# Optimization experiments

Hardware: AMD Instinct MI355X
Metric: run time of the kernel (lower is better)

The kernel has to match this reference:

```python
import jax, jax.numpy as jnp
import numpy as np

B, S, D, H = 1, 2048, 768, 12
HD = D // H


def layer_norm(x, g, b, eps=1e-5):
    mu = x.mean(-1, keepdims=True)
    var = ((x - mu) ** 2).mean(-1, keepdims=True)
    return (x - mu) * jax.lax.rsqrt(var + eps) * g + b


def setup_inputs() -> dict:
    key = jax.random.key(0)
    ks = jax.random.split(key, 16)
    s = 0.02
    exp_encodings = jax.random.normal(ks[0], (B, S, D), dtype=jnp.float32)
    pert_encodings = jax.random.normal(ks[1], (B, S, D), dtype=jnp.float32)
    adj = (jax.random.uniform(ks[2], (S, S)) < 0.01).astype(jnp.int32)
    adj = adj.at[jnp.arange(S), jnp.arange(S)].set(1)
    in_proj_w = jax.random.normal(ks[3], (3 * D, D)) * s
    in_proj_b = jnp.zeros((3 * D,), jnp.float32)
    out_proj_w = jax.random.normal(ks[4], (D, D)) * s
    out_proj_b = jnp.zeros((D,), jnp.float32)
    ln0_g = jnp.ones((D,), jnp.float32); ln0_b = jnp.zeros((D,), jnp.float32)
    ln1_g = jnp.ones((D,), jnp.float32); ln1_b = jnp.zeros((D,), jnp.float32)
    ln2_g = jnp.ones((D,), jnp.float32); ln2_b = jnp.zeros((D,), jnp.float32)
    w1 = jax.random.normal(ks[5], (D // 2, D)) * s
    b1 = jnp.zeros((D // 2,), jnp.float32)
    w2 = jax.random.normal(ks[6], (D, D // 2)) * s
    b2 = jnp.zeros((D,), jnp.float32)
    return dict(exp_encodings=exp_encodings, pert_encodings=pert_encodings,
                in_proj_w=in_proj_w, in_proj_b=in_proj_b,
                out_proj_w=out_proj_w, out_proj_b=out_proj_b,
                ln0_g=ln0_g, ln0_b=ln0_b, ln1_g=ln1_g, ln1_b=ln1_b,
                ln2_g=ln2_g, ln2_b=ln2_b, w1=w1, b1=b1, w2=w2, b2=b2,
                adj=adj)


def reference(exp_encodings, pert_encodings, in_proj_w, in_proj_b,
              out_proj_w, out_proj_b, ln0_g, ln0_b, ln1_g, ln1_b,
              ln2_g, ln2_b, w1, b1, w2, b2, adj):
    b, s, d = exp_encodings.shape
    hd = d // H
    # additive mask: 0 where edge, -inf elsewhere (diag guaranteed edge)
    mask = jnp.where(adj > 0, 0.0, -jnp.inf).astype(exp_encodings.dtype)
    x_in = layer_norm(exp_encodings + pert_encodings, ln0_g, ln0_b)
    # torch MultiheadAttention (batch_first) self-attention
    qkv = x_in @ in_proj_w.T + in_proj_b          # [b,s,3d]
    q, k, v = jnp.split(qkv, 3, axis=-1)
    q = q.reshape(b, s, H, hd)
    k = k.reshape(b, s, H, hd)
    v = v.reshape(b, s, H, hd)
    scores = jnp.einsum('bqhe,bkhe->bhqk', q, k) / np.sqrt(hd) + mask
    attn = jax.nn.softmax(scores, axis=-1)
    o = jnp.einsum('bhqk,bkhe->bqhe', attn, v).reshape(b, s, d)
    o = o @ out_proj_w.T + out_proj_b
    x = layer_norm(o + x_in, ln1_g, ln1_b)
    ff = jax.nn.relu(x @ w1.T + b1) @ w2.T + b2
    return layer_norm(x + ff, ln2_g, ln2_b)
```

## Files before the change

kernel.cpp:

```cpp
#include <hip/hip_runtime.h>

#define S 2048
#define D 768
#define NH 12
#define HD 64
#define TD (3 * D)

typedef __bf16 bf16_t;
typedef __bf16 v8bf __attribute__((ext_vector_type(8)));
typedef __bf16 v4bf __attribute__((ext_vector_type(4)));
typedef float v4f __attribute__((ext_vector_type(4)));

__device__ __forceinline__ float wave_reduce_sum(float v) {
#pragma unroll
    for (int o = 32; o > 0; o >>= 1) v += __shfl_down(v, o, 64);
    return v;
}
__device__ float block_reduce_sum(float v) {
    __shared__ float t4[4];
    int lane = threadIdx.x & 63, wid = threadIdx.x >> 6;
    v = wave_reduce_sum(v);
    __syncthreads();
    if (lane == 0) t4[wid] = v;
    __syncthreads();
    return t4[0] + t4[1] + t4[2] + t4[3];
}

#define NW0 (TD * D / 4)
#define NW1 (D * D / 4)
#define NW2 ((D / 2) * D / 4)
#define NW3 (D * (D / 2) / 4)
#define NWALL (NW0 + NW1 + NW2 + NW3)

__global__ __launch_bounds__(256) void addln_cvt(const float* __restrict__ A, const float* __restrict__ Bv,
                                                 const float* __restrict__ g, const float* __restrict__ be,
                                                 bf16_t* __restrict__ out,
                                                 const float* __restrict__ s0, const float* __restrict__ s1,
                                                 const float* __restrict__ s2, const float* __restrict__ s3,
                                                 bf16_t* __restrict__ d0, bf16_t* __restrict__ d1,
                                                 bf16_t* __restrict__ d2, bf16_t* __restrict__ d3) {
    int blk = blockIdx.x, t = threadIdx.x;
    if (blk >= S) {
        int i = (blk - S) * 256 + t;
        const float* sp; bf16_t* dp;
        if (i < NW0) { sp = s0; dp = d0; }
        else if (i < NW0 + NW1) { sp = s1; dp = d1; i -= NW0; }
        else if (i < NW0 + NW1 + NW2) { sp = s2; dp = d2; i -= NW0 + NW1; }
        else if (i < NWALL) { sp = s3; dp = d3; i -= NW0 + NW1 + NW2; }
        else return;
        float4 v = ((const float4*)sp)[i];
        v4bf o = {(bf16_t)v.x, (bf16_t)v.y, (bf16_t)v.z, (bf16_t)v.w};
        *(v4bf*)(dp + (size_t)i * 4) = o;
        return;
    }
    int row = blk;
    const float* a = A + (size_t)row * D;
    const float* b = Bv + (size_t)row * D;
    float x[3];
    float s = 0.f;
#pragma unroll
    for (int i = 0; i < 3; ++i) { int c = t + 256 * i; x[i] = a[c] + b[c]; s += x[i]; }
    float mean = block_reduce_sum(s) * (1.0f / D);
    float vs = 0.f;
#pragma unroll
    for (int i = 0; i < 3; ++i) { float d = x[i] - mean; vs += d * d; }
    float var = block_reduce_sum(vs) * (1.0f / D);
    float rstd = rsqrtf(var + 1e-5f);
#pragma unroll
    for (int i = 0; i < 3; ++i) {
        int c = t + 256 * i;
        out[(size_t)row * D + c] = (bf16_t)((x[i] - mean) * rstd * g[c] + be[c]);
    }
}

template <typename TO>
__global__ __launch_bounds__(256) void ln_only(const bf16_t* __restrict__ X,
                                               const float* __restrict__ g, const float* __restrict__ be,
                                               TO* __restrict__ out) {
    int row = blockIdx.x, t = threadIdx.x;
    const bf16_t* a = X + (size_t)row * D;
    float x[3];
    float s = 0.f;
#pragma unroll
    for (int i = 0; i < 3; ++i) { int c = t + 256 * i; x[i] = (float)a[c]; s += x[i]; }
    float mean = block_reduce_sum(s) * (1.0f / D);
    float vs = 0.f;
#pragma unroll
    for (int i = 0; i < 3; ++i) { float d = x[i] - mean; vs += d * d; }
    float var = block_reduce_sum(vs) * (1.0f / D);
    float rstd = rsqrtf(var + 1e-5f);
#pragma unroll
    for (int i = 0; i < 3; ++i) {
        int c = t + 256 * i;
        out[(size_t)row * D + c] = (TO)((x[i] - mean) * rstd * g[c] + be[c]);
    }
}

#define GBK 64

template <int TM, int TN, int RELU, bool RESID>
__global__ __launch_bounds__(256) void gemm_mfma(const bf16_t* __restrict__ A, const bf16_t* __restrict__ B,
                                                 const float* __restrict__ bias,
                                                 const bf16_t* __restrict__ Rsd, bf16_t* __restrict__ C,
                                                 int M, int N, int K) {
    constexpr int CA = TM * 8;
    constexpr int CHUNKS = (TM + TN) * 8;
    constexpr int P = CHUNKS / 256;
    static_assert(CHUNKS % 256 == 0, "chunk passes must be exact");
    constexpr int MI = TM / 32, NI = TN / 32;
    __shared__ bf16_t As[TM * GBK];
    __shared__ bf16_t Bs[TN * GBK];
    const int t = threadIdx.x;
    const int lane = t & 63, wave = t >> 6;
    const int wr = (wave >> 1) * (TM / 2), wc = (wave & 1) * (TN / 2);
    const int m0 = blockIdx.y * TM, n0 = blockIdx.x * TN;
    const int lm = lane & 15, q = lane >> 4;

    const bf16_t* gsrc[P];
    bf16_t* ldst[P];
#pragma unroll
    for (int p = 0; p < P; ++p) {
        int c = t + 256 * p;
        if (c < CA) {
            int slab = c / (TM * 4), r4 = c % (TM * 4);
            int row = r4 >> 2, c4 = r4 & 3;
            gsrc[p] = A + (size_t)(m0 + row) * K + slab * 32 + c4 * 8;
            ldst[p] = As + slab * (TM * 32) + row * 32 + c4 * 8;
        } else {
            int cc = c - CA;
            int slab = cc / (TN * 4), r4 = cc % (TN * 4);
            int row = r4 >> 2, c4 = r4 & 3;
            gsrc[p] = B + (size_t)(n0 + row) * K + slab * 32 + c4 * 8;
            ldst[p] = Bs + slab * (TN * 32) + row * 32 + c4 * 8;
        }
    }

    v4f acc[MI][NI] = {};

    for (int k0 = 0; k0 < K; k0 += GBK) {
#pragma unroll
        for (int p = 0; p < P; ++p)
            __builtin_amdgcn_global_load_lds((const __attribute__((address_space(1))) void*)(gsrc[p] + k0),
                                             (__attribute__((address_space(3))) void*)ldst[p], 16, 0, 0);
        __syncthreads();

        v8bf af[2][MI], bfr[2][NI];
#pragma unroll
        for (int s = 0; s < 2; ++s) {
#pragma unroll
            for (int i = 0; i < MI; ++i)
                af[s][i] = *(const v8bf*)(As + s * (TM * 32) + (wr + i * 16 + lm) * 32 + q * 8);
#pragma unroll
            for (int j = 0; j < NI; ++j)
                bfr[s][j] = *(const v8bf*)(Bs + s * (TN * 32) + (wc + j * 16 + lm) * 32 + q * 8);
        }
#pragma unroll
        for (int s = 0; s < 2; ++s)
#pragma unroll
            for (int i = 0; i < MI; ++i)
#pragma unroll
                for (int j = 0; j < NI; ++j)
                    acc[i][j] = __builtin_amdgcn_mfma_f32_16x16x32_bf16(af[s][i], bfr[s][j], acc[i][j], 0, 0, 0);
        __syncthreads();
    }

#pragma unroll
    for (int i = 0; i < MI; ++i)
#pragma unroll
        for (int j = 0; j < NI; ++j) {
            int col = n0 + wc + j * 16 + lm;
            float bs = bias[col];
#pragma unroll
            for (int r = 0; r < 4; ++r) {
                int row = m0 + wr + i * 16 + q * 4 + r;
                float v = acc[i][j][r] + bs;
                if (RELU) v = fmaxf(v, 0.f);
                if (RESID) v += (float)Rsd[(size_t)row * N + col];
                C[(size_t)row * N + col] = (bf16_t)v;
            }
        }
}

__global__ __launch_bounds__(256) void attn_sparse(const bf16_t* __restrict__ qkv, const int* __restrict__ adj,
                                                   bf16_t* __restrict__ O) {
    __shared__ int s_idx[128];
    __shared__ int s_cnt;
    __shared__ float s_q[D];
    __shared__ float s_p[NH][128];

    const int row = blockIdx.x, t = threadIdx.x;
    const int lane = t & 63, wave = t >> 6;
    if (t == 0) s_cnt = 0;
    __syncthreads();

    const int4* arow = (const int4*)(adj + (size_t)row * S);
#pragma unroll
    for (int p = 0; p < 2; ++p) {
        int4 v = arow[t + 256 * p];
        int base = (t + 256 * p) * 4;
        if (v.x) { int k = atomicAdd(&s_cnt, 1); if (k < 128) s_idx[k] = base + 0; }
        if (v.y) { int k = atomicAdd(&s_cnt, 1); if (k < 128) s_idx[k] = base + 1; }
        if (v.z) { int k = atomicAdd(&s_cnt, 1); if (k < 128) s_idx[k] = base + 2; }
        if (v.w) { int k = atomicAdd(&s_cnt, 1); if (k < 128) s_idx[k] = base + 3; }
    }
    for (int c = t; c < D; c += 256) s_q[c] = (float)qkv[(size_t)row * TD + c];
    __syncthreads();
    const int n = (s_cnt < 128) ? s_cnt : 128;

    for (int it = t; it < n * NH; it += 256) {
        int h = it / n, i = it - h * n;
        int j = s_idx[i];
        const bf16_t* kp = qkv + (size_t)j * TD + D + h * HD;
        const float* qp = s_q + h * HD;
        float dot = 0.f;
#pragma unroll
        for (int c = 0; c < HD; c += 8) {
            v8bf kv = *(const v8bf*)(kp + c);
#pragma unroll
            for (int e = 0; e < 8; ++e) dot += qp[c + e] * (float)kv[e];
        }
        s_p[h][i] = dot * 0.125f;
    }
    __syncthreads();

    for (int h = wave; h < NH; h += 4) {
        float v0 = (lane < n) ? s_p[h][lane] : -1e30f;
        float v1 = (lane + 64 < n) ? s_p[h][lane + 64] : -1e30f;
        float m = fmaxf(v0, v1);
#pragma unroll
        for (int o = 32; o > 0; o >>= 1) m = fmaxf(m, __shfl_xor(m, o, 64));
        float p0 = (lane < n) ? __expf(v0 - m) : 0.f;
        float p1 = (lane + 64 < n) ? __expf(v1 - m) : 0.f;
        float sm = p0 + p1;
#pragma unroll
        for (int o = 32; o > 0; o >>= 1) sm += __shfl_xor(sm, o, 64);
        float inv = 1.f / sm;
        if (lane < n) s_p[h][lane] = p0 * inv;
        if (lane + 64 < n) s_p[h][lane + 64] = p1 * inv;
    }
    __syncthreads();

    for (int o = t; o < D; o += 256) {
        int h = o >> 6, e = o & 63;
        const float* pp = s_p[h];
        float acc = 0.f;
        for (int i = 0; i < n; ++i)
            acc += pp[i] * (float)qkv[(size_t)s_idx[i] * TD + 2 * D + h * HD + e];
        O[(size_t)row * D + o] = (bf16_t)acc;
    }
}

extern "C" void kernel_launch(void* const* d_in, const int* in_sizes, int n_in,
                              void* d_out, int out_size, void* d_ws, size_t ws_size,
                              hipStream_t stream) {
    const float* exp_e = (const float*)d_in[0];
    const float* pert  = (const float*)d_in[1];
    const float* w_in  = (const float*)d_in[2];
    const float* b_in  = (const float*)d_in[3];
    const float* w_out = (const float*)d_in[4];
    const float* b_out = (const float*)d_in[5];
    const float* g0  = (const float*)d_in[6];
    const float* be0 = (const float*)d_in[7];
    const float* g1  = (const float*)d_in[8];
    const float* be1 = (const float*)d_in[9];
    const float* g2  = (const float*)d_in[10];
    const float* be2 = (const float*)d_in[11];
    const float* w1  = (const float*)d_in[12];
    const float* b1  = (const float*)d_in[13];
    const float* w2  = (const float*)d_in[14];
    const float* b2  = (const float*)d_in[15];
    const int*   adj = (const int*)d_in[16];
    float* out = (float*)d_out;

    const size_t SD = (size_t)S * D;
    bf16_t* wb_in  = (bf16_t*)d_ws;
    bf16_t* wb_out = wb_in + (size_t)TD * D;
    bf16_t* wb_1   = wb_out + (size_t)D * D;
    bf16_t* wb_2   = wb_1 + (size_t)(D / 2) * D;
    bf16_t* x_in   = wb_2 + (size_t)D * (D / 2);
    bf16_t* qkv    = x_in + SD;
    bf16_t* attn_o = qkv + 3 * SD;
    bf16_t* y1     = attn_o + SD;
    bf16_t* x1     = y1 + SD;
    bf16_t* ffh    = x1 + SD;
    bf16_t* y2     = ffh + SD / 2;

    const int CVTB = (NWALL + 255) / 256;
    addln_cvt<<<S + CVTB, 256, 0, stream>>>(exp_e, pert, g0, be0, x_in,
                                            w_in, w_out, w1, w2, wb_in, wb_out, wb_1, wb_2);
    gemm_mfma<64, 128, 0, false><<<dim3(TD / 128, S / 64), 256, 0, stream>>>(x_in, wb_in, b_in, nullptr, qkv, S, TD, D);
    attn_sparse<<<S, 256, 0, stream>>>(qkv, adj, attn_o);
    gemm_mfma<64, 64, 0, true><<<dim3(D / 64, S / 64), 256, 0, stream>>>(attn_o, wb_out, b_out, x_in, y1, S, D, D);
    ln_only<bf16_t><<<S, 256, 0, stream>>>(y1, g1, be1, x1);
    gemm_mfma<32, 64, 1, false><<<dim3((D / 2) / 64, S / 32), 256, 0, stream>>>(x1, wb_1, b1, nullptr, ffh, S, D / 2, D);
    gemm_mfma<64, 64, 0, true><<<dim3(D / 64, S / 64), 256, 0, stream>>>(ffh, wb_2, b2, x1, y2, S, D, D / 2);
    ln_only<float><<<S, 256, 0, stream>>>(y2, g2, be2, out);
}
```

Baseline: 196.3 us.

## Fuse LayerNorm into FF1 GEMM and unroll sparse attention dot/accumulate loops

Adds a kernel that computes LayerNorm of each 32-row tile directly into shared memory and then runs the first feed-forward GEMM with ReLU from that tile. This removes the separate ln_only launch and the reload of x1 from global memory. Only the blockIdx.x==0 column of blocks writes x1 out for the residual. The cost is that the LayerNorm is recomputed in each of the six N-tile blocks. The sparse attention kernel also gets vectorized float4 q loads in the QK dot and four independent accumulators in the PV gather, to expose more memory-level parallelism.

After: 203.6 us. 3.7% more time.

```diff
diff --git a/kernel.cpp b/kernel.cpp
--- a/kernel.cpp
+++ b/kernel.cpp
@@ -181,6 +181,96 @@
         }
 }
 
+#define FTM 32
+#define FTN 64
+#define FK  768
+#define FN  384
+
+__global__ __launch_bounds__(256) void ff1_ln_gemm(const bf16_t* __restrict__ y1,
+                                                   const float* __restrict__ g, const float* __restrict__ be,
+                                                   const bf16_t* __restrict__ B, const float* __restrict__ bias,
+                                                   bf16_t* __restrict__ x1g, bf16_t* __restrict__ Cffh) {
+    __shared__ bf16_t x1s[24 * 32 * 32];
+    __shared__ bf16_t Bs[FTN * GBK];
+    const int t = threadIdx.x, lane = t & 63, wave = t >> 6;
+    const int m0 = blockIdx.y * FTM, n0 = blockIdx.x * FTN;
+    const int lm = lane & 15, q = lane >> 4;
+
+#pragma unroll
+    for (int rr = 0; rr < 8; ++rr) {
+        int row = wave * 8 + rr;
+        const bf16_t* yp = y1 + (size_t)(m0 + row) * D;
+        float v[12];
+        float s = 0.f, s2 = 0.f;
+#pragma unroll
+        for (int e = 0; e < 12; ++e) {
+            v[e] = (float)yp[lane + 64 * e];
+            s += v[e]; s2 += v[e] * v[e];
+        }
+#pragma unroll
+        for (int o = 32; o > 0; o >>= 1) { s += __shfl_xor(s, o, 64); s2 += __shfl_xor(s2, o, 64); }
+        float mean = s * (1.0f / D);
+        float var = s2 * (1.0f / D) - mean * mean;
+        float rstd = rsqrtf(var + 1e-5f);
+#pragma unroll
+        for (int e = 0; e < 12; ++e) {
+            int c = lane + 64 * e;
+            bf16_t xv = (bf16_t)((v[e] - mean) * rstd * g[c] + be[c]);
+            x1s[(c >> 5) * 1024 + row * 32 + (c & 31)] = xv;
+            if (blockIdx.x == 0) x1g[(size_t)(m0 + row) * D + c] = xv;
+        }
+    }
+    __syncthreads();
+
+    const bf16_t* gsrc[2];
+    bf16_t* ldst[2];
+#pragma unroll
+    for (int p = 0; p < 2; ++p) {
+        int c = t + 256 * p;
+        int slab = c >> 8, r4 = c & 255;
+        int row = r4 >> 2, c4 = r4 & 3;
+        gsrc[p] = B + (size_t)(n0 + row) * FK + slab * 32 + c4 * 8;
+        ldst[p] = Bs + slab * (FTN * 32) + row * 32 + c4 * 8;
+    }
+
+    v4f acc[2] = {};
+    const int wr = (wave >> 1) * 16, wc = (wave & 1) * 32;
+
+    for (int k0 = 0; k0 < FK; k0 += GBK) {
+#pragma unroll
+        for (int p = 0; p < 2; ++p)
+            __builtin_amdgcn_global_load_lds((const __attribute__((address_space(1))) void*)(gsrc[p] + k0),
+                                             (__attribute__((address_space(3))) void*)ldst[p], 16, 0, 0);
+        __syncthreads();
+
+        v8bf af[2], bfr[2][2];
+#pragma unroll
+        for (int s = 0; s < 2; ++s) {
+            af[s] = *(const v8bf*)(x1s + ((k0 >> 5) + s) * 1024 + (wr + lm) * 32 + q * 8);
+#pragma unroll
+            for (int j = 0; j < 2; ++j)
+                bfr[s][j] = *(const v8bf*)(Bs + s * (FTN * 32) + (wc + j * 16 + lm) * 32 + q * 8);
+        }
+#pragma unroll
+        for (int s = 0; s < 2; ++s)
+#pragma unroll
+            for (int j = 0; j < 2; ++j)
+                acc[j] = __builtin_amdgcn_mfma_f32_16x16x32_bf16(af[s], bfr[s][j], acc[j], 0, 0, 0);
+        __syncthreads();
+    }
+
+#pragma unroll
+    for (int j = 0; j < 2; ++j) {
+        int col = n0 + wc + j * 16 + lm;
+        float bs = bias[col];
+#pragma unroll
+        for (int r = 0; r < 4; ++r) {
+            int row = m0 + wr + q * 4 + r;
+            Cffh[(size_t)row * FN + col] = (bf16_t)fmaxf(acc[j][r] + bs, 0.f);
+        }
+    }
+}
+
 __global__ __launch_bounds__(256) void attn_sparse(const bf16_t* __restrict__ qkv, const int* __restrict__ adj,
                                                    bf16_t* __restrict__ O) {
     __shared__ int s_idx[128];
@@ -210,14 +300,15 @@
     for (int it = t; it < n * NH; it += 256) {
         int h = it / n, i = it - h * n;
         int j = s_idx[i];
-        const bf16_t* kp = qkv + (size_t)j * TD + D + h * HD;
-        const float* qp = s_q + h * HD;
+        const v8bf* kp = (const v8bf*)(qkv + (size_t)j * TD + D + h * HD);
+        const float4* qp = (const float4*)(s_q + h * HD);
         float dot = 0.f;
 #pragma unroll
-        for (int c = 0; c < HD; c += 8) {
-            v8bf kv = *(const v8bf*)(kp + c);
-#pragma unroll
-            for (int e = 0; e < 8; ++e) dot += qp[c + e] * (float)kv[e];
+        for (int c = 0; c < 8; ++c) {
+            v8bf kv = kp[c];
+            float4 qa = qp[2 * c], qb = qp[2 * c + 1];
+            dot += qa.x * (float)kv[0] + qa.y * (float)kv[1] + qa.z * (float)kv[2] + qa.w * (float)kv[3]
+                 + qb.x * (float)kv[4] + qb.y * (float)kv[5] + qb.z * (float)kv[6] + qb.w * (float)kv[7];
         }
         s_p[h][i] = dot * 0.125f;
     }
@@ -243,10 +334,18 @@
     for (int o = t; o < D; o += 256) {
         int h = o >> 6, e = o & 63;
         const float* pp = s_p[h];
-        float acc = 0.f;
-        for (int i = 0; i < n; ++i)
-            acc += pp[i] * (float)qkv[(size_t)s_idx[i] * TD + 2 * D + h * HD + e];
-        O[(size_t)row * D + o] = (bf16_t)acc;
+        const bf16_t* vbase = qkv + 2 * D + h * HD + e;
+        float a0 = 0.f, a1 = 0.f, a2 = 0.f, a3 = 0.f;
+        int i = 0;
+        for (; i + 4 <= n; i += 4) {
+            int j0 = s_idx[i], j1 = s_idx[i + 1], j2 = s_idx[i + 2], j3 = s_idx[i + 3];
+            a0 += pp[i]     * (float)vbase[(size_t)j0 * TD];
+            a1 += pp[i + 1] * (float)vbase[(size_t)j1 * TD];
+            a2 += pp[i + 2] * (float)vbase[(size_t)j2 * TD];
+            a3 += pp[i + 3] * (float)vbase[(size_t)j3 * TD];
+        }
+        for (; i < n; ++i) a0 += pp[i] * (float)vbase[(size_t)s_idx[i] * TD];
+        O[(size_t)row * D + o] = (bf16_t)((a0 + a1) + (a2 + a3));
     }
 }
 
@@ -291,8 +390,7 @@
     gemm_mfma<64, 128, 0, false><<<dim3(TD / 128, S / 64), 256, 0, stream>>>(x_in, wb_in, b_in, nullptr, qkv, S, TD, D);
     attn_sparse<<<S, 256, 0, stream>>>(qkv, adj, attn_o);
     gemm_mfma<64, 64, 0, true><<<dim3(D / 64, S / 64), 256, 0, stream>>>(attn_o, wb_out, b_out, x_in, y1, S, D, D);
-    ln_only<bf16_t><<<S, 256, 0, stream>>>(y1, g1, be1, x1);
-    gemm_mfma<32, 64, 1, false><<<dim3((D / 2) / 64, S / 32), 256, 0, stream>>>(x1, wb_1, b1, nullptr, ffh, S, D / 2, D);
+    ff1_ln_gemm<<<dim3(FN / FTN, S / FTM), 256, 0, stream>>>(y1, g1, be1, wb_1, b1, x1, ffh);
     gemm_mfma<64, 64, 0, true><<<dim3(D / 64, S / 64), 256, 0, stream>>>(ffh, wb_2, b2, x1, y2, S, D, D / 2);
     ln_only<float><<<S, 256, 0, stream>>>(y2, g2, be2, out);
 }
```

## Replace tiled GEMM with B-resident kernel reading A from global, vectorize attention

Applied to the files above, without the earlier changes.

The shared-memory double-operand tiled GEMM is replaced by a kernel that loads a full 32-column slice of the weight matrix (all of K) into LDS once, then streams A fragments directly from global memory into MFMA with no per-K-step barriers. Each block covers CH*32 rows, so launch shapes change for all four GEMMs. The attention kernel also uses float4 loads of q in the score loop and four independent accumulators in the value gather to expose more memory-level parallelism. The cost is uncoalesced, uncached-in-LDS A reads that rely on L2 reuse across blocks, and large LDS per block for K=768 (48KB), which can limit occupancy.

New measurement: 255.2 us. 1.3x slower.

```diff
diff --git a/kernel.cpp b/kernel.cpp
--- a/kernel.cpp
+++ b/kernel.cpp
@@ -96,89 +96,56 @@
     }
 }
 
-#define GBK 64
-
-template <int TM, int TN, int RELU, bool RESID>
-__global__ __launch_bounds__(256) void gemm_mfma(const bf16_t* __restrict__ A, const bf16_t* __restrict__ B,
+template <int N, int K, int CH, int RELU, bool RESID>
+__global__ __launch_bounds__(256) void gemm_bres(const bf16_t* __restrict__ A, const bf16_t* __restrict__ B,
                                                  const float* __restrict__ bias,
-                                                 const bf16_t* __restrict__ Rsd, bf16_t* __restrict__ C,
-                                                 int M, int N, int K) {
-    constexpr int CA = TM * 8;
-    constexpr int CHUNKS = (TM + TN) * 8;
-    constexpr int P = CHUNKS / 256;
-    static_assert(CHUNKS % 256 == 0, "chunk passes must be exact");
-    constexpr int MI = TM / 32, NI = TN / 32;
-    __shared__ bf16_t As[TM * GBK];
-    __shared__ bf16_t Bs[TN * GBK];
-    const int t = threadIdx.x;
-    const int lane = t & 63, wave = t >> 6;
-    const int wr = (wave >> 1) * (TM / 2), wc = (wave & 1) * (TN / 2);
-    const int m0 = blockIdx.y * TM, n0 = blockIdx.x * TN;
+                                                 const bf16_t* __restrict__ Rsd, bf16_t* __restrict__ C) {
+    constexpr int SLABS = K / 32;
+    constexpr int PASSES = SLABS * 128 / 256;
+    __shared__ bf16_t Bs[SLABS * 1024];
+    const int t = threadIdx.x, lane = t & 63, wave = t >> 6;
+    const int wm = wave >> 1, wn = wave & 1;
     const int lm = lane & 15, q = lane >> 4;
-
-    const bf16_t* gsrc[P];
-    bf16_t* ldst[P];
-#pragma unroll
-    for (int p = 0; p < P; ++p) {
+    const int n0 = blockIdx.x * 32;
+    const int m0 = blockIdx.y * (CH * 32);
+
+#pragma unroll
+    for (int p = 0; p < PASSES; ++p) {
         int c = t + 256 * p;
-        if (c < CA) {
-            int slab = c / (TM * 4), r4 = c % (TM * 4);
-            int row = r4 >> 2, c4 = r4 & 3;
-            gsrc[p] = A + (size_t)(m0 + row) * K + slab * 32 + c4 * 8;
-            ldst[p] = As + slab * (TM * 32) + row * 32 + c4 * 8;
-        } else {
-            int cc = c - CA;
-            int slab = cc / (TN * 4), r4 = cc % (TN * 4);
-            int row = r4 >> 2, c4 = r4 & 3;
-            gsrc[p] = B + (size_t)(n0 + row) * K + slab * 32 + c4 * 8;
-            ldst[p] = Bs + slab * (TN * 32) + row * 32 + c4 * 8;
+        int slab = c >> 7, g = (c >> 5) & 3, r = c & 31;
+        __builtin_amdgcn_global_load_lds(
+            (const __attribute__((address_space(1))) void*)(B + (size_t)(n0 + r) * K + slab * 32 + g * 8),
+            (__attribute__((address_space(3))) void*)(Bs + c * 8), 16, 0, 0);
+    }
+    __syncthreads();
+
+    v4f acc[CH] = {};
+    const bf16_t* Ab = A + (size_t)(m0 + wm * 16 + lm) * K + q * 8;
+#pragma unroll 4
+    for (int slab = 0; slab < SLABS; ++slab) {
+        v8bf bfr = *(const v8bf*)(Bs + slab * 1024 + q * 256 + (wn * 16 + lm) * 8);
+        v8bf af[CH];
+#pragma unroll
+        for (int c = 0; c < CH; ++c)
+            af[c] = *(const v8bf*)(Ab + (size_t)(32 * c) * K + slab * 32);
+#pragma unroll
+        for (int c = 0; c < CH; ++c)
+            acc[c] = __builtin_amdgcn_mfma_f32_16x16x32_bf16(af[c], bfr, acc[c], 0, 0, 0);
+    }
+
+    const int col = n0 + wn * 16 + lm;
+    const float bb = bias[col];
+#pragma unroll
+    for (int c = 0; c < CH; ++c) {
+#pragma unroll
+        for (int r = 0; r < 4; ++r) {
+            int row = m0 + wm * 16 + 32 * c + q * 4 + r;
+            float v = acc[c][r] + bb;
+            if (RELU) v = fmaxf(v, 0.f);
+            if (RESID) v += (float)Rsd[(size_t)row * N + col];
+            C[(size_t)row * N + col] = (bf16_t)v;
         }
     }
-
-    v4f acc[MI][NI] = {};
-
-    for (int k0 = 0; k0 < K; k0 += GBK) {
-#pragma unroll
-        for (int p = 0; p < P; ++p)
-            __builtin_amdgcn_global_load_lds((const __attribute__((address_space(1))) void*)(gsrc[p] + k0),
-                                             (__attribute__((address_space(3))) void*)ldst[p], 16, 0, 0);
-        __syncthreads();
-
-        v8bf af[2][MI], bfr[2][NI];
-#pragma unroll
-        for (int s = 0; s < 2; ++s) {
-#pragma unroll
-            for (int i = 0; i < MI; ++i)
-                af[s][i] = *(const v8bf*)(As + s * (TM * 32) + (wr + i * 16 + lm) * 32 + q * 8);
-#pragma unroll
-            for (int j = 0; j < NI; ++j)
-                bfr[s][j] = *(const v8bf*)(Bs + s * (TN * 32) + (wc + j * 16 + lm) * 32 + q * 8);
-        }
-#pragma unroll
-        for (int s = 0; s < 2; ++s)
-#pragma unroll
-            for (int i = 0; i < MI; ++i)
-#pragma unroll
-                for (int j = 0; j < NI; ++j)
-                    acc[i][j] = __builtin_amdgcn_mfma_f32_16x16x32_bf16(af[s][i], bfr[s][j], acc[i][j], 0, 0, 0);
-        __syncthreads();
-    }
-
-#pragma unroll
-    for (int i = 0; i < MI; ++i)
-#pragma unroll
-        for (int j = 0; j < NI; ++j) {
-            int col = n0 + wc + j * 16 + lm;
-            float bs = bias[col];
-#pragma unroll
-            for (int r = 0; r < 4; ++r) {
-                int row = m0 + wr + i * 16 + q * 4 + r;
-                float v = acc[i][j][r] + bs;
-                if (RELU) v = fmaxf(v, 0.f);
-                if (RESID) v += (float)Rsd[(size_t)row * N + col];
-                C[(size_t)row * N + col] = (bf16_t)v;
-            }
-        }
 }
 
 __global__ __launch_bounds__(256) void attn_sparse(const bf16_t* __restrict__ qkv, const int* __restrict__ adj,
@@ -210,14 +177,15 @@
     for (int it = t; it < n * NH; it += 256) {
         int h = it / n, i = it - h * n;
         int j = s_idx[i];
-        const bf16_t* kp = qkv + (size_t)j * TD + D + h * HD;
-        const float* qp = s_q + h * HD;
+        const v8bf* kp = (const v8bf*)(qkv + (size_t)j * TD + D + h * HD);
+        const float4* qp = (const float4*)(s_q + h * HD);
         float dot = 0.f;
 #pragma unroll
-        for (int c = 0; c < HD; c += 8) {
-            v8bf kv = *(const v8bf*)(kp + c);
-#pragma unroll
-            for (int e = 0; e < 8; ++e) dot += qp[c + e] * (float)kv[e];
+        for (int c = 0; c < 8; ++c) {
+            v8bf kv = kp[c];
+            float4 qa = qp[2 * c], qb = qp[2 * c + 1];
+            dot += qa.x * (float)kv[0] + qa.y * (float)kv[1] + qa.z * (float)kv[2] + qa.w * (float)kv[3]
+                 + qb.x * (float)kv[4] + qb.y * (float)kv[5] + qb.z * (float)kv[6] + qb.w * (float)kv[7];
         }
         s_p[h][i] = dot * 0.125f;
     }
@@ -243,10 +211,18 @@
     for (int o = t; o < D; o += 256) {
         int h = o >> 6, e = o & 63;
         const float* pp = s_p[h];
-        float acc = 0.f;
-        for (int i = 0; i < n; ++i)
-            acc += pp[i] * (float)qkv[(size_t)s_idx[i] * TD + 2 * D + h * HD + e];
-        O[(size_t)row * D + o] = (bf16_t)acc;
+        const bf16_t* vbase = qkv + 2 * D + h * HD + e;
+        float a0 = 0.f, a1 = 0.f, a2 = 0.f, a3 = 0.f;
+        int i = 0;
+        for (; i + 4 <= n; i += 4) {
+            int j0 = s_idx[i], j1 = s_idx[i + 1], j2 = s_idx[i + 2], j3 = s_idx[i + 3];
+            a0 += pp[i]     * (float)vbase[(size_t)j0 * TD];
+            a1 += pp[i + 1] * (float)vbase[(size_t)j1 * TD];
+            a2 += pp[i + 2] * (float)vbase[(size_t)j2 * TD];
+            a3 += pp[i + 3] * (float)vbase[(size_t)j3 * TD];
+        }
+        for (; i < n; ++i) a0 += pp[i] * (float)vbase[(size_t)s_idx[i] * TD];
+        O[(size_t)row * D + o] = (bf16_t)((a0 + a1) + (a2 + a3));
     }
 }
 
@@ -288,11 +264,11 @@
     const int CVTB = (NWALL + 255) / 256;
     addln_cvt<<<S + CVTB, 256, 0, stream>>>(exp_e, pert, g0, be0, x_in,
                                             w_in, w_out, w1, w2, wb_in, wb_out, wb_1, wb_2);
-    gemm_mfma<64, 128, 0, false><<<dim3(TD / 128, S / 64), 256, 0, stream>>>(x_in, wb_in, b_in, nullptr, qkv, S, TD, D);
+    gemm_bres<TD, D, 4, 0, false><<<dim3(TD / 32, S / 128), 256, 0, stream>>>(x_in, wb_in, b_in, nullptr, qkv);
     attn_sparse<<<S, 256, 0, stream>>>(qkv, adj, attn_o);
-    gemm_mfma<64, 64, 0, true><<<dim3(D / 64, S / 64), 256, 0, stream>>>(attn_o, wb_out, b_out, x_in, y1, S, D, D);
+    gemm_bres<D, D, 2, 0, true><<<dim3(D / 32, S / 64), 256, 0, stream>>>(attn_o, wb_out, b_out, x_in, y1);
     ln_only<bf16_t><<<S, 256, 0, stream>>>(y1, g1, be1, x1);
-    gemm_mfma<32, 64, 1, false><<<dim3((D / 2) / 64, S / 32), 256, 0, stream>>>(x1, wb_1, b1, nullptr, ffh, S, D / 2, D);
-    gemm_mfma<64, 64, 0, true><<<dim3(D / 64, S / 64), 256, 0, stream>>>(ffh, wb_2, b2, x1, y2, S, D, D / 2);
+    gemm_bres<D / 2, D, 2, 1, false><<<dim3((D / 2) / 32, S / 64), 256, 0, stream>>>(x1, wb_1, b1, nullptr, ffh);
+    gemm_bres<D, D / 2, 2, 0, true><<<dim3(D / 32, S / 64), 256, 0, stream>>>(ffh, wb_2, b2, x1, y2);
     ln_only<float><<<S, 256, 0, stream>>>(y2, g2, be2, out);
 }
```

## Build adjacency index lists in the first kernel and unroll sparse attention loops

Applied to the files above, without the earlier changes.

The per-row scan of the adjacency matrix moves out of the attention kernel into extra blocks of the first LayerNorm/convert kernel, which write a compact index list and count per row to workspace. The attention kernel then loads only the prepared indices, so it no longer reads a 2048-int row of the mask while the QKV data sits in cache. The QK dot product now reads q with float4 loads, and the PV loop uses four independent accumulators to raise memory-level parallelism on the gathered V loads. The cost is extra workspace and more blocks in the first launch.

Result: slower. 201.8 us (+2.8%).

```diff
diff --git a/kernel.cpp b/kernel.cpp
--- a/kernel.cpp
+++ b/kernel.cpp
@@ -31,6 +31,7 @@
 #define NW2 ((D / 2) * D / 4)
 #define NW3 (D * (D / 2) / 4)
 #define NWALL (NW0 + NW1 + NW2 + NW3)
+#define CVTB ((NWALL + 255) / 256)
 
 __global__ __launch_bounds__(256) void addln_cvt(const float* __restrict__ A, const float* __restrict__ Bv,
                                                  const float* __restrict__ g, const float* __restrict__ be,
@@ -38,8 +39,32 @@
                                                  const float* __restrict__ s0, const float* __restrict__ s1,
                                                  const float* __restrict__ s2, const float* __restrict__ s3,
                                                  bf16_t* __restrict__ d0, bf16_t* __restrict__ d1,
-                                                 bf16_t* __restrict__ d2, bf16_t* __restrict__ d3) {
+                                                 bf16_t* __restrict__ d2, bf16_t* __restrict__ d3,
+                                                 const int* __restrict__ adj,
+                                                 int* __restrict__ csr_cnt, int* __restrict__ csr_idx) {
     int blk = blockIdx.x, t = threadIdx.x;
+    if (blk >= S + CVTB) {
+        __shared__ int sc_idx[128];
+        __shared__ int sc_cnt;
+        int row = blk - S - CVTB;
+        if (t == 0) sc_cnt = 0;
+        __syncthreads();
+        const int4* arow = (const int4*)(adj + (size_t)row * S);
+#pragma unroll
+        for (int p = 0; p < 2; ++p) {
+            int4 v = arow[t + 256 * p];
+            int base = (t + 256 * p) * 4;
+            if (v.x) { int k = atomicAdd(&sc_cnt, 1); if (k < 128) sc_idx[k] = base + 0; }
+            if (v.y) { int k = atomicAdd(&sc_cnt, 1); if (k < 128) sc_idx[k] = base + 1; }
+            if (v.z) { int k = atomicAdd(&sc_cnt, 1); if (k < 128) sc_idx[k] = base + 2; }
+            if (v.w) { int k = atomicAdd(&sc_cnt, 1); if (k < 128) sc_idx[k] = base + 3; }
+        }
+        __syncthreads();
+        int n = (sc_cnt < 128) ? sc_cnt : 128;
+        if (t == 0) csr_cnt[row] = n;
+        if (t < n) csr_idx[(size_t)row * 128 + t] = sc_idx[t];
+        return;
+    }
     if (blk >= S) {
         int i = (blk - S) * 256 + t;
         const float* sp; bf16_t* dp;
@@ -181,43 +206,34 @@
         }
 }
 
-__global__ __launch_bounds__(256) void attn_sparse(const bf16_t* __restrict__ qkv, const int* __restrict__ adj,
+__global__ __launch_bounds__(256) void attn_sparse(const bf16_t* __restrict__ qkv,
+                                                   const int* __restrict__ csr_cnt,
+                                                   const int* __restrict__ csr_idx,
                                                    bf16_t* __restrict__ O) {
     __shared__ int s_idx[128];
-    __shared__ int s_cnt;
     __shared__ float s_q[D];
     __shared__ float s_p[NH][128];
 
     const int row = blockIdx.x, t = threadIdx.x;
     const int lane = t & 63, wave = t >> 6;
-    if (t == 0) s_cnt = 0;
-    __syncthreads();
-
-    const int4* arow = (const int4*)(adj + (size_t)row * S);
-#pragma unroll
-    for (int p = 0; p < 2; ++p) {
-        int4 v = arow[t + 256 * p];
-        int base = (t + 256 * p) * 4;
-        if (v.x) { int k = atomicAdd(&s_cnt, 1); if (k < 128) s_idx[k] = base + 0; }
-        if (v.y) { int k = atomicAdd(&s_cnt, 1); if (k < 128) s_idx[k] = base + 1; }
-        if (v.z) { int k = atomicAdd(&s_cnt, 1); if (k < 128) s_idx[k] = base + 2; }
-        if (v.w) { int k = atomicAdd(&s_cnt, 1); if (k < 128) s_idx[k] = base + 3; }
-    }
+    const int n = csr_cnt[row];
+
+    if (t < n) s_idx[t] = csr_idx[(size_t)row * 128 + t];
     for (int c = t; c < D; c += 256) s_q[c] = (float)qkv[(size_t)row * TD + c];
     __syncthreads();
-    const int n = (s_cnt < 128) ? s_cnt : 128;
 
     for (int it = t; it < n * NH; it += 256) {
         int h = it / n, i = it - h * n;
         int j = s_idx[i];
-        const bf16_t* kp = qkv + (size_t)j * TD + D + h * HD;
-        const float* qp = s_q + h * HD;
+        const v8bf* kp = (const v8bf*)(qkv + (size_t)j * TD + D + h * HD);
+        const float4* qp = (const float4*)(s_q + h * HD);
         float dot = 0.f;
 #pragma unroll
-        for (int c = 0; c < HD; c += 8) {
-            v8bf kv = *(const v8bf*)(kp + c);
-#pragma unroll
-            for (int e = 0; e < 8; ++e) dot += qp[c + e] * (float)kv[e];
+        for (int c = 0; c < 8; ++c) {
+            v8bf kv = kp[c];
+            float4 qa = qp[2 * c], qb = qp[2 * c + 1];
+            dot += qa.x * (float)kv[0] + qa.y * (float)kv[1] + qa.z * (float)kv[2] + qa.w * (float)kv[3]
+                 + qb.x * (float)kv[4] + qb.y * (float)kv[5] + qb.z * (float)kv[6] + qb.w * (float)kv[7];
         }
         s_p[h][i] = dot * 0.125f;
     }
@@ -243,10 +259,18 @@
     for (int o = t; o < D; o += 256) {
         int h = o >> 6, e = o & 63;
         const float* pp = s_p[h];
-        float acc = 0.f;
-        for (int i = 0; i < n; ++i)
-            acc += pp[i] * (float)qkv[(size_t)s_idx[i] * TD + 2 * D + h * HD + e];
-        O[(size_t)row * D + o] = (bf16_t)acc;
+        const bf16_t* vbase = qkv + 2 * D + h * HD + e;
+        float a0 = 0.f, a1 = 0.f, a2 = 0.f, a3 = 0.f;
+        int i = 0;
+        for (; i + 4 <= n; i += 4) {
+            int j0 = s_idx[i], j1 = s_idx[i + 1], j2 = s_idx[i + 2], j3 = s_idx[i + 3];
+            a0 += pp[i]     * (float)vbase[(size_t)j0 * TD];
+            a1 += pp[i + 1] * (float)vbase[(size_t)j1 * TD];
+            a2 += pp[i + 2] * (float)vbase[(size_t)j2 * TD];
+            a3 += pp[i + 3] * (float)vbase[(size_t)j3 * TD];
+        }
+        for (; i < n; ++i) a0 += pp[i] * (float)vbase[(size_t)s_idx[i] * TD];
+        O[(size_t)row * D + o] = (bf16_t)((a0 + a1) + (a2 + a3));
     }
 }
 
@@ -284,12 +308,14 @@
     bf16_t* x1     = y1 + SD;
     bf16_t* ffh    = x1 + SD;
     bf16_t* y2     = ffh + SD / 2;
-
-    const int CVTB = (NWALL + 255) / 256;
-    addln_cvt<<<S + CVTB, 256, 0, stream>>>(exp_e, pert, g0, be0, x_in,
-                                            w_in, w_out, w1, w2, wb_in, wb_out, wb_1, wb_2);
+    int* csr_cnt   = (int*)(y2 + SD);
+    int* csr_idx   = csr_cnt + S;
+
+    addln_cvt<<<S + CVTB + S, 256, 0, stream>>>(exp_e, pert, g0, be0, x_in,
+                                                w_in, w_out, w1, w2, wb_in, wb_out, wb_1, wb_2,
+                                                adj, csr_cnt, csr_idx);
     gemm_mfma<64, 128, 0, false><<<dim3(TD / 128, S / 64), 256, 0, stream>>>(x_in, wb_in, b_in, nullptr, qkv, S, TD, D);
-    attn_sparse<<<S, 256, 0, stream>>>(qkv, adj, attn_o);
+    attn_sparse<<<S, 256, 0, stream>>>(qkv, csr_cnt, csr_idx, attn_o);
     gemm_mfma<64, 64, 0, true><<<dim3(D / 64, S / 64), 256, 0, stream>>>(attn_o, wb_out, b_out, x_in, y1, S, D, D);
     ln_only<bf16_t><<<S, 256, 0, stream>>>(y1, g1, be1, x1);
     gemm_mfma<32, 64, 1, false><<<dim3((D / 2) / 64, S / 32), 256, 0, stream>>>(x1, wb_1, b1, nullptr, ffh, S, D / 2, D);
```
